# Kernel optimization log

Measured on AMD Instinct MI355X. Metric: run time of the kernel, lower is better.

Reference implementation:

```python
import jax, jax.numpy as jnp
import numpy as np

B, H, D = 2048, 50, 400          # batch, history_length, news/category embed dim
S, C = 285, 18                   # num_subcategories, num_categories
NC = 50                          # num_clicks_embed_dim (= history_length table size)
FILL = 1e-30                     # masked_fill value used by the original module


def setup_inputs() -> dict:
    key = jax.random.key(0)
    ks = jax.random.split(key, 9)
    vectors = jax.random.normal(ks[0], (B, H, D), dtype=jnp.float32)
    subcategory = jax.random.randint(ks[1], (B, H), 0, S, dtype=jnp.int32)
    category = jax.random.randint(ks[2], (B, H), 0, C, dtype=jnp.int32)
    subcat_embed = jax.random.normal(ks[3], (S, D), dtype=jnp.float32) * 0.02
    cat_embed = jax.random.normal(ks[4], (C, D), dtype=jnp.float32) * 0.02
    clicks_embed = jax.random.normal(ks[5], (H, NC), dtype=jnp.float32) * 0.02
    w_news = jax.random.normal(ks[6], (D,), dtype=jnp.float32) * 0.05
    w_subcat = jax.random.normal(ks[7], (D + NC,), dtype=jnp.float32) * 0.05
    w_cat = jax.random.normal(ks[8], (D + NC,), dtype=jnp.float32) * 0.05
    return {"vectors": vectors, "subcategory": subcategory, "category": category,
            "subcat_embed": subcat_embed, "cat_embed": cat_embed,
            "clicks_embed": clicks_embed, "w_news": w_news,
            "w_subcat": w_subcat, "w_cat": w_cat}


def reference(vectors, subcategory, category, subcat_embed, cat_embed,
              clicks_embed, w_news, w_subcat, w_cat):
    sub_mask = jax.nn.one_hot(subcategory, S, dtype=vectors.dtype)   # [B,H,S]
    cat_mask = jax.nn.one_hot(category, C, dtype=vectors.dtype)      # [B,H,C]
    sub_to_cat = jnp.einsum('bhs,bhc->bsc', sub_mask, cat_mask)      # [B,S,C]

    # --- news -> subcategory attention pooling ---
    news_scores = jnp.einsum('bhd,d->bh', vectors, w_news)           # [B,H]
    scores = jnp.where(sub_mask > 0, news_scores[:, :, None], FILL)  # [B,H,S]
    news_w = jax.nn.softmax(scores, axis=1)
    sub_news_repr = jnp.einsum('bhs,bhd->bsd', news_w, vectors)      # [B,S,D]
    sub_repr = sub_news_repr + subcat_embed[None]                    # [B,S,D]

    sub_clicks = sub_mask.sum(axis=1)                                # [B,S] float counts
    sub_weights = sub_clicks / sub_clicks.sum(axis=1, keepdims=True)
    sub_clicks_emb = clicks_embed[sub_clicks.astype(jnp.int32)]      # [B,S,NC]

    # --- subcategory -> category attention pooling ---
    sc_scores = jnp.einsum('bsk,k->bs',
                           jnp.concatenate([sub_repr, sub_clicks_emb], axis=2),
                           w_subcat)                                 # [B,S]
    scores2 = jnp.where(sub_to_cat > 0, sc_scores[:, :, None], FILL) # [B,S,C]
    sub_w = jax.nn.softmax(scores2, axis=1)
    cat_sub_repr = jnp.einsum('bsc,bsd->bcd', sub_w, sub_repr)       # [B,C,D]
    cat_repr = cat_sub_repr + cat_embed[None]                        # [B,C,D]

    cat_clicks = cat_mask.sum(axis=1)                                # [B,C]
    cat_weights = cat_clicks / cat_clicks.sum(axis=1, keepdims=True)
    cat_clicks_emb = clicks_embed[cat_clicks.astype(jnp.int32)]      # [B,C,NC]

    # --- category -> user attention pooling (unmasked) ---
    c_scores = jnp.einsum('bck,k->bc',
                          jnp.concatenate([cat_repr, cat_clicks_emb], axis=2),
                          w_cat)                                     # [B,C]
    cat_w = jax.nn.softmax(c_scores, axis=1)
    user_repr = jnp.einsum('bc,bcd->bd', cat_w, cat_repr)            # [B,D]

    return (sub_repr, sub_weights, cat_repr, cat_weights, user_repr)
```

## Files before the change

kernel.cpp:

```cpp
#include <hip/hip_runtime.h>

#define BB 2048
#define HH 50
#define DD 400
#define D4 100
#define SS 285
#define CC 18
#define NCC 50
#define FILLV 1e-30f

static constexpr int BLOCK = 512;
static constexpr int TOT4 = SS * D4;

static constexpr size_t OFF1 = (size_t)BB * SS * DD;
static constexpr size_t OFF2 = OFF1 + (size_t)BB * SS;
static constexpr size_t OFF3 = OFF2 + (size_t)BB * CC * DD;
static constexpr size_t OFF4 = OFF3 + (size_t)BB * CC;

#define WS_ETOT 0
#define WS_SCE  400
#define WS_CEDS 685
#define WS_CEDC 735

__device__ __forceinline__ float4 f4fma(float a, float4 b, float4 c) {
    return make_float4(fmaf(a, b.x, c.x), fmaf(a, b.y, c.y), fmaf(a, b.z, c.z), fmaf(a, b.w, c.w));
}
__device__ __forceinline__ float4 f4scale(float4 a, float s) {
    return make_float4(a.x * s, a.y * s, a.z * s, a.w * s);
}
__device__ __forceinline__ float4 f4add(float4 a, float4 b) {
    return make_float4(a.x + b.x, a.y + b.y, a.z + b.z, a.w + b.w);
}

__global__ void hierec_pre(const float* __restrict__ subcat_embed,
                           const float* __restrict__ clicks_embed,
                           const float* __restrict__ w_subcat,
                           const float* __restrict__ w_cat,
                           float* __restrict__ ws)
{
    const int tid = threadIdx.x;
    const int lane = tid & 63;
    const int wave = tid >> 6;
    const int wpb = blockDim.x >> 6;
    const int gw = blockIdx.x * wpb + wave;
    const int nw = gridDim.x * wpb;

    for (int s = gw; s < SS; s += nw) {
        float p = 0.f;
        for (int d = lane; d < DD; d += 64) p += subcat_embed[s * DD + d] * w_subcat[d];
        for (int off = 32; off; off >>= 1) p += __shfl_down(p, off);
        if (lane == 0) ws[WS_SCE + s] = p;
    }
    if (blockIdx.x == 0) {
        for (int d = tid; d < DD; d += blockDim.x) {
            float a = 0.f;
            for (int s = 0; s < SS; ++s) a += subcat_embed[s * DD + d];
            ws[WS_ETOT + d] = a;
        }
    }
    if (blockIdx.x == 1) {
        for (int k = wave; k < HH; k += wpb) {
            float p1 = 0.f, p2 = 0.f;
            if (lane < NCC) {
                float v = clicks_embed[k * NCC + lane];
                p1 = v * w_subcat[DD + lane];
                p2 = v * w_cat[DD + lane];
            }
            for (int off = 32; off; off >>= 1) {
                p1 += __shfl_down(p1, off);
                p2 += __shfl_down(p2, off);
            }
            if (lane == 0) { ws[WS_CEDS + k] = p1; ws[WS_CEDC + k] = p2; }
        }
    }
}

__global__ __launch_bounds__(BLOCK) void hierec_main(
    const float* __restrict__ vectors,
    const int*   __restrict__ subcategory,
    const int*   __restrict__ category,
    const float* __restrict__ subcat_embed,
    const float* __restrict__ cat_embed,
    const float* __restrict__ w_news,
    const float* __restrict__ w_subcat,
    const float* __restrict__ w_cat,
    const float* __restrict__ pre,
    float* __restrict__ out)
{
    const int b    = blockIdx.x;
    const int tid  = threadIdx.x;
    const int lane = tid & 63;
    const int wave = tid >> 6;

    __shared__ float  catbuf[CC][DD];
    __shared__ float4 vt4L[D4];
    __shared__ float4 et4L[D4];
    __shared__ float  coefS[SS];
    __shared__ unsigned long long maskS[SS];
    __shared__ int    cntS[SS];
    __shared__ float  ns1L[HH], ns2L[HH], uL[HH], ZL[HH], scL[HH], wNL[HH];
    __shared__ unsigned long long maskL[HH];
    __shared__ int    hsL[HH], hcL[HH], repL[HH], prepL[HH];
    __shared__ float  GmL[CC][HH];
    __shared__ float  mcL[CC], ucL[CC], rZcL[CC], AL[CC], csL[CC], catwL[CC];
    __shared__ int    cntcL[CC];
    __shared__ int    prepCL[HH], prepSL[HH], prepJL[HH];
    __shared__ float  prepGL[HH];
    __shared__ int    npL;
    __shared__ float  PvL;

    const float*  vb  = vectors + (size_t)b * HH * DD;
    const float4* vb4 = (const float4*)vb;
    const float4* se4 = (const float4*)subcat_embed;

    if (tid < HH) {
        hsL[tid] = subcategory[b * HH + tid];
        hcL[tid] = category[b * HH + tid];
    }
    for (int s = tid; s < SS; s += BLOCK) {
        coefS[s] = 1.f / (float)HH;
        maskS[s] = 0ull;
        cntS[s]  = 0;
    }
    for (int h = wave; h < HH; h += 8) {
        float p1 = 0.f, p2 = 0.f;
        for (int d = lane; d < DD; d += 64) {
            float v = vb[h * DD + d];
            p1 += v * w_news[d];
            p2 += v * w_subcat[d];
        }
        for (int off = 32; off; off >>= 1) {
            p1 += __shfl_down(p1, off);
            p2 += __shfl_down(p2, off);
        }
        if (lane == 0) { ns1L[h] = p1; ns2L[h] = p2; }
    }
    if (tid < DD) {
        float a = 0.f;
        for (int h = 0; h < HH; ++h) a += vb[h * DD + tid];
        ((float*)vt4L)[tid] = a;
        ((float*)et4L)[tid] = pre[WS_ETOT + tid];
    }
    __syncthreads();

    if (tid < HH) {
        const int h = tid;
        const int s = hsL[h], c = hcL[h];
        unsigned long long mask = 0ull, pmask = 0ull;
        for (int j = 0; j < HH; ++j) {
            bool ms = (hsL[j] == s);
            mask  |= (unsigned long long)(ms ? 1 : 0) << j;
            pmask |= (unsigned long long)((ms && hcL[j] == c) ? 1 : 0) << j;
        }
        int cnt = __popcll(mask);
        bool rep = ((__ffsll((long long)mask) - 1) == h);

        float m = FILLV;
        unsigned long long t = mask;
        while (t) { int j = __ffsll((long long)t) - 1; t &= t - 1; m = fmaxf(m, ns1L[j]); }
        float u = expf(FILLV - m);
        float sumE = 0.f, sum2 = 0.f;
        t = mask;
        while (t) {
            int j = __ffsll((long long)t) - 1; t &= t - 1;
            float e = expf(ns1L[j] - m);
            sumE += e;
            sum2 += (e - u) * ns2L[j];
        }
        float Z = sumE + (float)(HH - cnt) * u;
        float vt2 = 0.f;
        for (int j = 0; j < HH; ++j) vt2 += ns2L[j];
        int ci = cnt < (NCC - 1) ? cnt : (NCC - 1);
        float sc = (sum2 + u * vt2) / Z + pre[WS_SCE + s] + pre[WS_CEDS + ci];

        float e_h = expf(ns1L[h] - m);
        wNL[h] = (e_h - u) / Z;
        uL[h] = u; ZL[h] = Z; maskL[h] = mask; scL[h] = sc;
        repL[h]  = rep ? 1 : 0;
        prepL[h] = ((__ffsll((long long)pmask) - 1) == h) ? 1 : 0;
        if (rep) { coefS[s] = u / Z; maskS[s] = mask; cntS[s] = cnt; }
    }
    __syncthreads();

    if (tid < CC) {
        const int c = tid;
        float mc = FILLV; int n = 0, cc2 = 0;
        for (int j = 0; j < HH; ++j) {
            if (hcL[j] == c) ++cc2;
            if (prepL[j] && hcL[j] == c) { ++n; mc = fmaxf(mc, scL[j]); }
        }
        float u = expf(FILLV - mc);
        float sumE = 0.f;
        for (int j = 0; j < HH; ++j)
            if (prepL[j] && hcL[j] == c) sumE += expf(scL[j] - mc);
        float Zc = sumE + (float)(SS - n) * u;
        mcL[c] = mc; ucL[c] = u; rZcL[c] = 1.f / Zc; cntcL[c] = cc2;
        out[OFF3 + (size_t)b * CC + c] = (float)cc2 / (float)HH;
    }
    if (tid == 64) {
        int nd = 0, np = 0;
        float sumUb = 0.f;
        for (int j = 0; j < HH; ++j) {
            if (repL[j]) { ++nd; sumUb += uL[j] / ZL[j]; }
            if (prepL[j]) { prepCL[np] = hcL[j]; prepSL[np] = hsL[j]; prepJL[np] = j; ++np; }
        }
        npL = np;
        PvL = (float)(SS - nd) / (float)HH + sumUb;
    }
    for (int s = tid; s < SS; s += BLOCK)
        out[OFF1 + (size_t)b * SS + s] = (float)cntS[s] / (float)HH;
    __syncthreads();

    for (int idx = tid; idx < CC * HH; idx += BLOCK) {
        int c = idx / HH, h = idx - c * HH;
        bool exists = false;
        unsigned long long t = maskL[h];
        while (t) {
            int k = __ffsll((long long)t) - 1; t &= t - 1;
            if (hcL[k] == c) { exists = true; break; }
        }
        float g = exists ? (expf(scL[h] - mcL[c]) - ucL[c]) : 0.f;
        GmL[c][h] = wNL[h] * (ucL[c] + g);
    }
    if (tid < CC) {
        const int c = tid;
        float A = ucL[c] * PvL;
        for (int j = 0; j < HH; ++j)
            if (prepL[j] && hcL[j] == c)
                A += (expf(scL[j] - mcL[c]) - ucL[c]) * (uL[j] / ZL[j]);
        AL[c] = A;
    }
    for (int jj = tid; jj < npL; jj += BLOCK) {
        int j = prepJL[jj], c = prepCL[jj];
        prepGL[jj] = expf(scL[j] - mcL[c]) - ucL[c];
    }
    __syncthreads();

    {
        float4* o4 = (float4*)(out + (size_t)b * SS * DD);
        for (int i = tid; i < TOT4; i += BLOCK) {
            int s = i / D4;
            int q = i - s * D4;
            float4 e4  = se4[(size_t)s * D4 + q];
            float4 acc = f4scale(vt4L[q], coefS[s]);
            unsigned long long t = maskS[s];
            while (t) {
                int j = __ffsll((long long)t) - 1; t &= t - 1;
                acc = f4fma(wNL[j], vb4[j * D4 + q], acc);
            }
            o4[i] = f4add(acc, e4);
        }
    }

    {
        const int c0 = wave, c1 = wave + 8, c2 = wave + 16;
        const bool has2 = (c2 < CC);
        const int np = npL;
        for (int d4 = lane; d4 < D4; d4 += 64) {
            float4 vt = vt4L[d4], et = et4L[d4];
            float4 a0 = f4fma(ucL[c0], et, f4scale(vt, AL[c0]));
            float4 a1 = f4fma(ucL[c1], et, f4scale(vt, AL[c1]));
            float4 a2 = has2 ? f4fma(ucL[c2], et, f4scale(vt, AL[c2]))
                             : make_float4(0.f, 0.f, 0.f, 0.f);
            for (int h = 0; h < HH; ++h) {
                float4 v = vb4[h * D4 + d4];
                a0 = f4fma(GmL[c0][h], v, a0);
                a1 = f4fma(GmL[c1][h], v, a1);
                if (has2) a2 = f4fma(GmL[c2][h], v, a2);
            }
            for (int jj = 0; jj < np; ++jj) {
                int pc = prepCL[jj];
                if (pc == c0 || pc == c1 || (has2 && pc == c2)) {
                    float4 e = se4[(size_t)prepSL[jj] * D4 + d4];
                    float g = prepGL[jj];
                    if (pc == c0) a0 = f4fma(g, e, a0);
                    else if (pc == c1) a1 = f4fma(g, e, a1);
                    else a2 = f4fma(g, e, a2);
                }
            }
            const float4* ce4 = (const float4*)cat_embed;
            float4* ocat = (float4*)(out + OFF2 + (size_t)b * CC * DD);
            float4 v0 = f4add(f4scale(a0, rZcL[c0]), ce4[c0 * D4 + d4]);
            float4 v1 = f4add(f4scale(a1, rZcL[c1]), ce4[c1 * D4 + d4]);
            ((float4*)&catbuf[c0][0])[d4] = v0;
            ((float4*)&catbuf[c1][0])[d4] = v1;
            ocat[c0 * D4 + d4] = v0;
            ocat[c1 * D4 + d4] = v1;
            if (has2) {
                float4 v2 = f4add(f4scale(a2, rZcL[c2]), ce4[c2 * D4 + d4]);
                ((float4*)&catbuf[c2][0])[d4] = v2;
                ocat[c2 * D4 + d4] = v2;
            }
        }
    }
    __syncthreads();

    for (int c = wave; c < CC; c += 8) {
        float p = 0.f;
        for (int d = lane; d < DD; d += 64) p += catbuf[c][d] * w_cat[d];
        for (int off = 32; off; off >>= 1) p += __shfl_down(p, off);
        if (lane == 0) {
            int ci = cntcL[c] < (NCC - 1) ? cntcL[c] : (NCC - 1);
            csL[c] = p + pre[WS_CEDC + ci];
        }
    }
    __syncthreads();

    if (tid < CC) {
        float m = csL[0];
        for (int j = 1; j < CC; ++j) m = fmaxf(m, csL[j]);
        float Zc = 0.f;
        for (int j = 0; j < CC; ++j) Zc += expf(csL[j] - m);
        catwL[tid] = expf(csL[tid] - m) / Zc;
    }
    __syncthreads();
    if (tid < DD) {
        float a = 0.f;
        for (int c = 0; c < CC; ++c) a += catwL[c] * catbuf[c][tid];
        out[OFF4 + (size_t)b * DD + tid] = a;
    }
}

extern "C" void kernel_launch(void* const* d_in, const int* in_sizes, int n_in,
                              void* d_out, int out_size, void* d_ws, size_t ws_size,
                              hipStream_t stream) {
    const float* vectors      = (const float*)d_in[0];
    const int*   subcategory  = (const int*)d_in[1];
    const int*   category     = (const int*)d_in[2];
    const float* subcat_embed = (const float*)d_in[3];
    const float* cat_embed    = (const float*)d_in[4];
    const float* clicks_embed = (const float*)d_in[5];
    const float* w_news       = (const float*)d_in[6];
    const float* w_subcat     = (const float*)d_in[7];
    const float* w_cat        = (const float*)d_in[8];
    float* out = (float*)d_out;
    float* ws  = (float*)d_ws;

    hipLaunchKernelGGL(hierec_pre, dim3(32), dim3(256), 0, stream,
                       subcat_embed, clicks_embed, w_subcat, w_cat, ws);
    hipLaunchKernelGGL(hierec_main, dim3(BB), dim3(BLOCK), 0, stream,
                       vectors, subcategory, category, subcat_embed, cat_embed,
                       w_news, w_subcat, w_cat, ws, out);
}
```

Baseline: 592.8 us.

## Compute category scores algebraically and drop catbuf, halve block, nontemporal stores

The category scores are now derived algebraically from per-history dot products with w_cat and precomputed embedding·w_cat terms, so cat_repr no longer has to be materialized in shared memory before the softmax. user_repr is rebuilt directly from vectors and the embeddings using combined weights. This removes the 28KB catbuf, which should let more blocks reside per CU. The block size drops to 256 with a launch-bounds occupancy hint, and output writes use nontemporal stores. The price is recomputing user_repr with an extra pass over vectors and embeddings, and a small change in floating-point rounding order.

After: 585.3 us. About the same (-1.3%).

```diff
diff --git a/kernel.cpp b/kernel.cpp
--- a/kernel.cpp
+++ b/kernel.cpp
@@ -9,7 +9,7 @@
 #define NCC 50
 #define FILLV 1e-30f
 
-static constexpr int BLOCK = 512;
+static constexpr int BLOCK = 256;
 static constexpr int TOT4 = SS * D4;
 
 static constexpr size_t OFF1 = (size_t)BB * SS * DD;
@@ -19,37 +19,39 @@
 
 #define WS_ETOT 0
 #define WS_SCE  400
-#define WS_CEDS 685
-#define WS_CEDC 735
-
-__device__ __forceinline__ float4 f4fma(float a, float4 b, float4 c) {
-    return make_float4(fmaf(a, b.x, c.x), fmaf(a, b.y, c.y), fmaf(a, b.z, c.z), fmaf(a, b.w, c.w));
-}
-__device__ __forceinline__ float4 f4scale(float4 a, float s) {
-    return make_float4(a.x * s, a.y * s, a.z * s, a.w * s);
-}
-__device__ __forceinline__ float4 f4add(float4 a, float4 b) {
-    return make_float4(a.x + b.x, a.y + b.y, a.z + b.z, a.w + b.w);
-}
+#define WS_SEW  688
+#define WS_CEDS 976
+#define WS_CEDC 1026
+#define WS_CEW  1076
+
+typedef float f4 __attribute__((ext_vector_type(4)));
 
 __global__ void hierec_pre(const float* __restrict__ subcat_embed,
+                           const float* __restrict__ cat_embed,
                            const float* __restrict__ clicks_embed,
                            const float* __restrict__ w_subcat,
                            const float* __restrict__ w_cat,
                            float* __restrict__ ws)
 {
-    const int tid = threadIdx.x;
+    const int tid  = threadIdx.x;
     const int lane = tid & 63;
     const int wave = tid >> 6;
-    const int wpb = blockDim.x >> 6;
-    const int gw = blockIdx.x * wpb + wave;
-    const int nw = gridDim.x * wpb;
+    const int wpb  = blockDim.x >> 6;
+    const int gw   = blockIdx.x * wpb + wave;
+    const int nw   = gridDim.x * wpb;
 
     for (int s = gw; s < SS; s += nw) {
-        float p = 0.f;
-        for (int d = lane; d < DD; d += 64) p += subcat_embed[s * DD + d] * w_subcat[d];
-        for (int off = 32; off; off >>= 1) p += __shfl_down(p, off);
-        if (lane == 0) ws[WS_SCE + s] = p;
+        float p1 = 0.f, p2 = 0.f;
+        for (int d = lane; d < DD; d += 64) {
+            float v = subcat_embed[s * DD + d];
+            p1 += v * w_subcat[d];
+            p2 += v * w_cat[d];
+        }
+        for (int off = 32; off; off >>= 1) {
+            p1 += __shfl_down(p1, off);
+            p2 += __shfl_down(p2, off);
+        }
+        if (lane == 0) { ws[WS_SCE + s] = p1; ws[WS_SEW + s] = p2; }
     }
     if (blockIdx.x == 0) {
         for (int d = tid; d < DD; d += blockDim.x) {
@@ -73,9 +75,17 @@
             if (lane == 0) { ws[WS_CEDS + k] = p1; ws[WS_CEDC + k] = p2; }
         }
     }
+    if (blockIdx.x == 2) {
+        for (int c = wave; c < CC; c += wpb) {
+            float p = 0.f;
+            for (int d = lane; d < DD; d += 64) p += cat_embed[c * DD + d] * w_cat[d];
+            for (int off = 32; off; off >>= 1) p += __shfl_down(p, off);
+            if (lane == 0) ws[WS_CEW + c] = p;
+        }
+    }
 }
 
-__global__ __launch_bounds__(BLOCK) void hierec_main(
+__global__ __launch_bounds__(BLOCK, 8) void hierec_main(
     const float* __restrict__ vectors,
     const int*   __restrict__ subcategory,
     const int*   __restrict__ category,
@@ -92,26 +102,27 @@
     const int lane = tid & 63;
     const int wave = tid >> 6;
 
-    __shared__ float  catbuf[CC][DD];
-    __shared__ float4 vt4L[D4];
-    __shared__ float4 et4L[D4];
+    __shared__ f4     vt4L[D4];
+    __shared__ f4     et4L[D4];
     __shared__ float  coefS[SS];
     __shared__ unsigned long long maskS[SS];
     __shared__ int    cntS[SS];
-    __shared__ float  ns1L[HH], ns2L[HH], uL[HH], ZL[HH], scL[HH], wNL[HH];
+    __shared__ float  ns1L[HH], ns2L[HH], ns3L[HH];
+    __shared__ float  uzL[HH], wNL[HH], scL[HH];
     __shared__ unsigned long long maskL[HH];
     __shared__ int    hsL[HH], hcL[HH], repL[HH], prepL[HH];
     __shared__ float  GmL[CC][HH];
     __shared__ float  mcL[CC], ucL[CC], rZcL[CC], AL[CC], csL[CC], catwL[CC];
     __shared__ int    cntcL[CC];
     __shared__ int    prepCL[HH], prepSL[HH], prepJL[HH];
-    __shared__ float  prepGL[HH];
+    __shared__ float  prepGL[HH], uPL[HH], uGL[HH];
     __shared__ int    npL;
-    __shared__ float  PvL;
-
-    const float*  vb  = vectors + (size_t)b * HH * DD;
-    const float4* vb4 = (const float4*)vb;
-    const float4* se4 = (const float4*)subcat_embed;
+    __shared__ float  PvL, vtwL, etwL, uAL, uEL;
+
+    const float* vb  = vectors + (size_t)b * HH * DD;
+    const f4*    vb4 = (const f4*)vb;
+    const f4*    se4 = (const f4*)subcat_embed;
+    const f4*    ce4 = (const f4*)cat_embed;
 
     if (tid < HH) {
         hsL[tid] = subcategory[b * HH + tid];
@@ -122,24 +133,29 @@
         maskS[s] = 0ull;
         cntS[s]  = 0;
     }
-    for (int h = wave; h < HH; h += 8) {
-        float p1 = 0.f, p2 = 0.f;
+    __syncthreads();
+
+    for (int h = wave; h < HH; h += 4) {
+        float p1 = 0.f, p2 = 0.f, p3 = 0.f;
         for (int d = lane; d < DD; d += 64) {
             float v = vb[h * DD + d];
             p1 += v * w_news[d];
             p2 += v * w_subcat[d];
+            p3 += v * w_cat[d];
         }
         for (int off = 32; off; off >>= 1) {
             p1 += __shfl_down(p1, off);
             p2 += __shfl_down(p2, off);
-        }
-        if (lane == 0) { ns1L[h] = p1; ns2L[h] = p2; }
-    }
-    if (tid < DD) {
-        float a = 0.f;
-        for (int h = 0; h < HH; ++h) a += vb[h * DD + tid];
-        ((float*)vt4L)[tid] = a;
-        ((float*)et4L)[tid] = pre[WS_ETOT + tid];
+            p3 += __shfl_down(p3, off);
+        }
+        if (lane == 0) { ns1L[h] = p1; ns2L[h] = p2; ns3L[h] = p3; }
+    }
+    if (tid < D4) {
+        f4 a = {0.f, 0.f, 0.f, 0.f};
+        #pragma unroll 5
+        for (int h = 0; h < HH; ++h) a += vb4[h * D4 + tid];
+        vt4L[tid] = a;
+        et4L[tid] = ((const f4*)pre)[tid];
     }
     __syncthreads();
 
@@ -174,11 +190,22 @@
         float sc = (sum2 + u * vt2) / Z + pre[WS_SCE + s] + pre[WS_CEDS + ci];
 
         float e_h = expf(ns1L[h] - m);
+        float uz = u / Z;
         wNL[h] = (e_h - u) / Z;
-        uL[h] = u; ZL[h] = Z; maskL[h] = mask; scL[h] = sc;
+        uzL[h] = uz; maskL[h] = mask; scL[h] = sc;
         repL[h]  = rep ? 1 : 0;
         prepL[h] = ((__ffsll((long long)pmask) - 1) == h) ? 1 : 0;
-        if (rep) { coefS[s] = u / Z; maskS[s] = mask; cntS[s] = cnt; }
+        if (rep) { coefS[s] = uz; maskS[s] = mask; cntS[s] = cnt; }
+    } else if (wave == 1) {
+        float p = 0.f;
+        const float* et = (const float*)et4L;
+        for (int d = lane; d < DD; d += 64) p += et[d] * w_cat[d];
+        for (int off = 32; off; off >>= 1) p += __shfl_down(p, off);
+        if (lane == 0) etwL = p;
+    } else if (wave == 2) {
+        float p = (lane < HH) ? ns3L[lane] : 0.f;
+        for (int off = 32; off; off >>= 1) p += __shfl_down(p, off);
+        if (lane == 0) vtwL = p;
     }
     __syncthreads();
 
@@ -195,20 +222,22 @@
             if (prepL[j] && hcL[j] == c) sumE += expf(scL[j] - mc);
         float Zc = sumE + (float)(SS - n) * u;
         mcL[c] = mc; ucL[c] = u; rZcL[c] = 1.f / Zc; cntcL[c] = cc2;
-        out[OFF3 + (size_t)b * CC + c] = (float)cc2 / (float)HH;
+        __builtin_nontemporal_store((float)cc2 * (1.f / (float)HH),
+                                    &out[OFF3 + (size_t)b * CC + c]);
     }
     if (tid == 64) {
         int nd = 0, np = 0;
         float sumUb = 0.f;
         for (int j = 0; j < HH; ++j) {
-            if (repL[j]) { ++nd; sumUb += uL[j] / ZL[j]; }
+            if (repL[j]) { ++nd; sumUb += uzL[j]; }
             if (prepL[j]) { prepCL[np] = hcL[j]; prepSL[np] = hsL[j]; prepJL[np] = j; ++np; }
         }
         npL = np;
-        PvL = (float)(SS - nd) / (float)HH + sumUb;
+        PvL = (float)(SS - nd) * (1.f / (float)HH) + sumUb;
     }
     for (int s = tid; s < SS; s += BLOCK)
-        out[OFF1 + (size_t)b * SS + s] = (float)cntS[s] / (float)HH;
+        __builtin_nontemporal_store((float)cntS[s] * (1.f / (float)HH),
+                                    &out[OFF1 + (size_t)b * SS + s]);
     __syncthreads();
 
     for (int idx = tid; idx < CC * HH; idx += BLOCK) {
@@ -227,82 +256,30 @@
         float A = ucL[c] * PvL;
         for (int j = 0; j < HH; ++j)
             if (prepL[j] && hcL[j] == c)
-                A += (expf(scL[j] - mcL[c]) - ucL[c]) * (uL[j] / ZL[j]);
+                A += (expf(scL[j] - mcL[c]) - ucL[c]) * uzL[j];
         AL[c] = A;
     }
-    for (int jj = tid; jj < npL; jj += BLOCK) {
-        int j = prepJL[jj], c = prepCL[jj];
-        prepGL[jj] = expf(scL[j] - mcL[c]) - ucL[c];
-    }
-    __syncthreads();
-
-    {
-        float4* o4 = (float4*)(out + (size_t)b * SS * DD);
-        for (int i = tid; i < TOT4; i += BLOCK) {
-            int s = i / D4;
-            int q = i - s * D4;
-            float4 e4  = se4[(size_t)s * D4 + q];
-            float4 acc = f4scale(vt4L[q], coefS[s]);
-            unsigned long long t = maskS[s];
-            while (t) {
-                int j = __ffsll((long long)t) - 1; t &= t - 1;
-                acc = f4fma(wNL[j], vb4[j * D4 + q], acc);
-            }
-            o4[i] = f4add(acc, e4);
-        }
-    }
-
-    {
-        const int c0 = wave, c1 = wave + 8, c2 = wave + 16;
-        const bool has2 = (c2 < CC);
+    __syncthreads();
+    if (tid >= 64 && tid < 64 + HH) {
+        int jj = tid - 64;
+        if (jj < npL) {
+            int j = prepJL[jj], c = prepCL[jj];
+            prepGL[jj] = expf(scL[j] - mcL[c]) - ucL[c];
+        }
+    }
+    __syncthreads();
+
+    if (tid < CC) {
+        const int c = tid;
+        float sG = 0.f;
+        for (int h = 0; h < HH; ++h) sG += GmL[c][h] * ns3L[h];
+        float sP = 0.f;
         const int np = npL;
-        for (int d4 = lane; d4 < D4; d4 += 64) {
-            float4 vt = vt4L[d4], et = et4L[d4];
-            float4 a0 = f4fma(ucL[c0], et, f4scale(vt, AL[c0]));
-            float4 a1 = f4fma(ucL[c1], et, f4scale(vt, AL[c1]));
-            float4 a2 = has2 ? f4fma(ucL[c2], et, f4scale(vt, AL[c2]))
-                             : make_float4(0.f, 0.f, 0.f, 0.f);
-            for (int h = 0; h < HH; ++h) {
-                float4 v = vb4[h * D4 + d4];
-                a0 = f4fma(GmL[c0][h], v, a0);
-                a1 = f4fma(GmL[c1][h], v, a1);
-                if (has2) a2 = f4fma(GmL[c2][h], v, a2);
-            }
-            for (int jj = 0; jj < np; ++jj) {
-                int pc = prepCL[jj];
-                if (pc == c0 || pc == c1 || (has2 && pc == c2)) {
-                    float4 e = se4[(size_t)prepSL[jj] * D4 + d4];
-                    float g = prepGL[jj];
-                    if (pc == c0) a0 = f4fma(g, e, a0);
-                    else if (pc == c1) a1 = f4fma(g, e, a1);
-                    else a2 = f4fma(g, e, a2);
-                }
-            }
-            const float4* ce4 = (const float4*)cat_embed;
-            float4* ocat = (float4*)(out + OFF2 + (size_t)b * CC * DD);
-            float4 v0 = f4add(f4scale(a0, rZcL[c0]), ce4[c0 * D4 + d4]);
-            float4 v1 = f4add(f4scale(a1, rZcL[c1]), ce4[c1 * D4 + d4]);
-            ((float4*)&catbuf[c0][0])[d4] = v0;
-            ((float4*)&catbuf[c1][0])[d4] = v1;
-            ocat[c0 * D4 + d4] = v0;
-            ocat[c1 * D4 + d4] = v1;
-            if (has2) {
-                float4 v2 = f4add(f4scale(a2, rZcL[c2]), ce4[c2 * D4 + d4]);
-                ((float4*)&catbuf[c2][0])[d4] = v2;
-                ocat[c2 * D4 + d4] = v2;
-            }
-        }
-    }
-    __syncthreads();
-
-    for (int c = wave; c < CC; c += 8) {
-        float p = 0.f;
-        for (int d = lane; d < DD; d += 64) p += catbuf[c][d] * w_cat[d];
-        for (int off = 32; off; off >>= 1) p += __shfl_down(p, off);
-        if (lane == 0) {
-            int ci = cntcL[c] < (NCC - 1) ? cntcL[c] : (NCC - 1);
-            csL[c] = p + pre[WS_CEDC + ci];
-        }
+        for (int jj = 0; jj < np; ++jj)
+            if (prepCL[jj] == c) sP += prepGL[jj] * pre[WS_SEW + prepSL[jj]];
+        int ci = cntcL[c] < (NCC - 1) ? cntcL[c] : (NCC - 1);
+        csL[c] = rZcL[c] * (AL[c] * vtwL + ucL[c] * etwL + sG + sP)
+                 + pre[WS_CEW + c] + pre[WS_CEDC + ci];
     }
     __syncthreads();
 
@@ -314,10 +291,70 @@
         catwL[tid] = expf(csL[tid] - m) / Zc;
     }
     __syncthreads();
-    if (tid < DD) {
-        float a = 0.f;
-        for (int c = 0; c < CC; ++c) a += catwL[c] * catbuf[c][tid];
-        out[OFF4 + (size_t)b * DD + tid] = a;
+    if (tid < HH) {
+        float g = 0.f;
+        for (int c = 0; c < CC; ++c) g += catwL[c] * rZcL[c] * GmL[c][tid];
+        uGL[tid] = g;
+    }
+    if (tid == 64) {
+        float uA = 0.f, uE = 0.f;
+        for (int c = 0; c < CC; ++c) {
+            uA += catwL[c] * rZcL[c] * AL[c];
+            uE += catwL[c] * rZcL[c] * ucL[c];
+        }
+        uAL = uA; uEL = uE;
+    }
+    if (tid >= 128 && tid < 128 + HH) {
+        int jj = tid - 128;
+        if (jj < npL) {
+            int c = prepCL[jj];
+            uPL[jj] = catwL[c] * rZcL[c] * prepGL[jj];
+        }
+    }
+    __syncthreads();
+
+
+    {
+        f4* oc = (f4*)(out + OFF2 + (size_t)b * CC * DD);
+        const int np = npL;
+        for (int i = tid; i < CC * D4; i += BLOCK) {
+            int c = i / D4, q = i - c * D4;
+            f4 acc = AL[c] * vt4L[q] + ucL[c] * et4L[q];
+            #pragma unroll 5
+            for (int h = 0; h < HH; ++h) acc += GmL[c][h] * vb4[h * D4 + q];
+            for (int jj = 0; jj < np; ++jj)
+                if (prepCL[jj] == c) acc += prepGL[jj] * se4[prepSL[jj] * D4 + q];
+            acc = rZcL[c] * acc + ce4[i];
+            __builtin_nontemporal_store(acc, &oc[i]);
+        }
+    }
+
+    {
+        f4* ou = (f4*)(out + OFF4 + (size_t)b * DD);
+        const int np = npL;
+        for (int q = tid; q < D4; q += BLOCK) {
+            f4 acc = uAL * vt4L[q] + uEL * et4L[q];
+            #pragma unroll 5
+            for (int h = 0; h < HH; ++h) acc += uGL[h] * vb4[h * D4 + q];
+            for (int jj = 0; jj < np; ++jj) acc += uPL[jj] * se4[prepSL[jj] * D4 + q];
+            for (int c = 0; c < CC; ++c) acc += catwL[c] * ce4[c * D4 + q];
+            __builtin_nontemporal_store(acc, &ou[q]);
+        }
+    }
+
+    {
+        f4* o4 = (f4*)(out + (size_t)b * SS * DD);
+        for (int i = tid; i < TOT4; i += BLOCK) {
+            int s = i / D4;
+            int q = i - s * D4;
+            f4 acc = coefS[s] * vt4L[q] + se4[i];
+            unsigned long long t = maskS[s];
+            while (t) {
+                int j = __ffsll((long long)t) - 1; t &= t - 1;
+                acc += wNL[j] * vb4[j * D4 + q];
+            }
+            __builtin_nontemporal_store(acc, &o4[i]);
+        }
     }
 }
 
@@ -337,7 +374,7 @@
     float* ws  = (float*)d_ws;
 
     hipLaunchKernelGGL(hierec_pre, dim3(32), dim3(256), 0, stream,
-                       subcat_embed, clicks_embed, w_subcat, w_cat, ws);
+                       subcat_embed, cat_embed, clicks_embed, w_subcat, w_cat, ws);
     hipLaunchKernelGGL(hierec_main, dim3(BB), dim3(BLOCK), 0, stream,
                        vectors, subcategory, category, subcat_embed, cat_embed,
                        w_news, w_subcat, w_cat, ws, out);
```
